# Kernel optimization log

Measured on AMD Instinct MI355X. Metric: run time of the kernel, lower is better.

The kernel has to match this reference:

```python
import jax, jax.numpy as jnp
import numpy as np

BS, SEQ, NV, DM, K = 128, 2048, 64, 512, 64
MAX_ITER, TOL = 10, 1e-4


def setup_inputs() -> dict:
    key = jax.random.key(0)
    k1, k2, k3, k4 = jax.random.split(key, 4)
    x = jax.random.normal(k1, (BS, SEQ, NV), jnp.float32)
    bound = 1.0 / np.sqrt(SEQ)
    W = jax.random.uniform(k2, (DM, SEQ), jnp.float32, -bound, bound)  # nn.Linear weight
    b = jax.random.uniform(k3, (DM,), jnp.float32, -bound, bound)
    centroids = jax.random.normal(k4, (K, DM), jnp.float32)  # kaiming-uniform-init param (random stand-in)
    return {"x": x, "W": W, "b": b, "centroids": centroids}


def _kmeans(x_emb, centroids):
    # x_emb: [N, DM]; fixed-length scan with a `done` flag emulating torch's tol break.
    N = x_emb.shape[0]
    x_sq = jnp.sum(x_emb * x_emb, axis=1, keepdims=True)  # [N,1]

    def body(state, _):
        cent, ids, done = state
        # squared euclidean distances (argmin-equivalent to cdist p=2)
        d2 = x_sq - 2.0 * (x_emb @ cent.T) + jnp.sum(cent * cent, axis=1)  # [N,K]
        new_ids = jnp.argmin(d2, axis=1)
        sums = jax.ops.segment_sum(x_emb, new_ids, num_segments=K)          # [K,DM]
        counts = jax.ops.segment_sum(jnp.ones((N,), x_emb.dtype), new_ids, num_segments=K)
        means = sums / jnp.maximum(counts, 1.0)[:, None]
        new_cent = jnp.where((counts > 0)[:, None], means, cent)  # empty cluster keeps old centroid
        shift = jnp.linalg.norm(new_cent - cent)
        cent_out = jnp.where(done, cent, new_cent)
        ids_out = jnp.where(done, ids, new_ids)
        done_out = done | (shift < TOL)
        return (cent_out, ids_out, done_out), None

    init = (centroids, jnp.zeros((N,), jnp.int32), jnp.array(False))
    (cent, ids, _), _ = jax.lax.scan(body, init, None, length=MAX_ITER)
    return ids, cent


def reference(x, W, b, centroids):
    # x: [bs, seq, n_vars] -> permute -> linear(seq->d_model) -> [bs*n_vars, d_model]
    xt = jnp.transpose(x, (0, 2, 1))                 # [bs, n_vars, seq]
    x_emb = (xt @ W.T + b).reshape(-1, DM)           # [bs*n_vars, d_model]
    ids, cent = _kmeans(x_emb, centroids)
    prob = jax.nn.one_hot(ids, K, dtype=jnp.float32).reshape(BS, NV, K)
    return prob, cent, x_emb
```

## Files before the change

kernel.cpp:

```cpp
#include <hip/hip_runtime.h>

#define SEQ 2048
#define NVAR 64
#define DMODEL 512
#define BSZ 128
#define KC 64
#define NPT (BSZ*NVAR)
#define MAXIT 10

typedef __bf16 bf16x8 __attribute__((ext_vector_type(8)));
typedef float f32x4 __attribute__((ext_vector_type(4)));

__device__ __forceinline__ void load_lds16(const void* g, void* l) {
  __builtin_amdgcn_global_load_lds((const __attribute__((address_space(1))) void*)g,
                                   (__attribute__((address_space(3))) void*)l, 16, 0, 0);
}

__device__ __forceinline__ unsigned short bf16_rn(float x) {
  unsigned int u = __float_as_uint(x);
  u += 0x7fffu + ((u >> 16) & 1u);
  return (unsigned short)(u >> 16);
}

__global__ __launch_bounds__(256) void prep_k(const float* __restrict__ x,
    unsigned short* __restrict__ Xh, unsigned short* __restrict__ Xl,
    const float* __restrict__ W, unsigned short* __restrict__ Wh,
    unsigned short* __restrict__ Wl) {
  __shared__ float tile[64 * 65];
  const int fid = blockIdx.x;
  const int t = threadIdx.x;

  if (fid < 1024) {
    int i = (fid * 256 + t) * 4;
    float4 v = *(const float4*)(W + i);
    ushort4 h, l;
    h.x = bf16_rn(v.x); l.x = bf16_rn(v.x - __uint_as_float((unsigned)h.x << 16));
    h.y = bf16_rn(v.y); l.y = bf16_rn(v.y - __uint_as_float((unsigned)h.y << 16));
    h.z = bf16_rn(v.z); l.z = bf16_rn(v.z - __uint_as_float((unsigned)h.z << 16));
    h.w = bf16_rn(v.w); l.w = bf16_rn(v.w - __uint_as_float((unsigned)h.w << 16));
    *(ushort4*)(Wh + i) = h;
    *(ushort4*)(Wl + i) = l;
  }

  const int k0 = (fid & 31) * 64;
  const int bs = fid >> 5;
  const float* xb = x + (size_t)bs * SEQ * NVAR + (size_t)k0 * NVAR;
  #pragma unroll
  for (int p = 0; p < 4; ++p) {
    int idx = t + 256 * p;
    int row = idx >> 4, c4 = (idx & 15) * 4;
    float4 v = *(const float4*)(xb + row * NVAR + c4);
    tile[row * 65 + c4 + 0] = v.x; tile[row * 65 + c4 + 1] = v.y;
    tile[row * 65 + c4 + 2] = v.z; tile[row * 65 + c4 + 3] = v.w;
  }
  __syncthreads();
  const int v = t >> 2;
  const int kc = (t & 3) * 16;
  unsigned short h[16], l[16];
  #pragma unroll
  for (int j = 0; j < 16; ++j) {
    float f = tile[(kc + j) * 65 + v];
    h[j] = bf16_rn(f);
    l[j] = bf16_rn(f - __uint_as_float((unsigned)h[j] << 16));
  }
  size_t off = (size_t)(bs * 64 + v) * SEQ + k0 + kc;
  *(uint4*)(Xh + off)     = *(uint4*)&h[0];
  *(uint4*)(Xh + off + 8) = *(uint4*)&h[8];
  *(uint4*)(Xl + off)     = *(uint4*)&l[0];
  *(uint4*)(Xl + off + 8) = *(uint4*)&l[8];
}

__global__ __launch_bounds__(256) void gemm_mfma(
    const unsigned short* __restrict__ Ah, const unsigned short* __restrict__ Al,
    const unsigned short* __restrict__ Bh, const unsigned short* __restrict__ Bl,
    const float* __restrict__ bias, float* __restrict__ emb) {
  __shared__ unsigned short sAh[32 * 64] __attribute__((aligned(16)));
  __shared__ unsigned short sAl[32 * 64] __attribute__((aligned(16)));
  __shared__ unsigned short sBh[256 * 64] __attribute__((aligned(16)));
  __shared__ unsigned short sBl[256 * 64] __attribute__((aligned(16)));
  const int t = threadIdx.x;
  const int w = t >> 6, lane = t & 63;
  const int m0 = blockIdx.x * 32;
  const int n0 = blockIdx.y * 256;
  const int wn = w * 64;
  const int lrow = lane >> 3, sl8 = lane & 7;
  const int csrc = sl8 ^ lrow;

  f32x4 acc[2][4];
  #pragma unroll
  for (int i = 0; i < 2; ++i)
    #pragma unroll
    for (int j = 0; j < 4; ++j) acc[i][j] = (f32x4){0.f, 0.f, 0.f, 0.f};

  for (int kt = 0; kt < SEQ; kt += 64) {
    __syncthreads();
    {
      const int r = w * 8 + lrow;
      const size_t ga = (size_t)(m0 + r) * SEQ + kt + csrc * 8;
      load_lds16(Ah + ga, &sAh[r * 64 + sl8 * 8]);
      load_lds16(Al + ga, &sAl[r * 64 + sl8 * 8]);
    }
    #pragma unroll
    for (int i = 0; i < 8; ++i) {
      const int r = w * 64 + i * 8 + lrow;
      const size_t gb = (size_t)(n0 + r) * SEQ + kt + csrc * 8;
      load_lds16(Bh + gb, &sBh[r * 64 + sl8 * 8]);
      load_lds16(Bl + gb, &sBl[r * 64 + sl8 * 8]);
    }
    __syncthreads();
    #pragma unroll
    for (int kk = 0; kk < 2; ++kk) {
      const int sl = ((kk * 4 + (lane >> 4)) ^ (lane & 7)) * 8;
      bf16x8 ah[2], al[2], bh[4], bl[4];
      #pragma unroll
      for (int mi = 0; mi < 2; ++mi) {
        int off = (mi * 16 + (lane & 15)) * 64 + sl;
        ah[mi] = *(const bf16x8*)&sAh[off];
        al[mi] = *(const bf16x8*)&sAl[off];
      }
      #pragma unroll
      for (int ni = 0; ni < 4; ++ni) {
        int off = (wn + ni * 16 + (lane & 15)) * 64 + sl;
        bh[ni] = *(const bf16x8*)&sBh[off];
        bl[ni] = *(const bf16x8*)&sBl[off];
      }
      #pragma unroll
      for (int mi = 0; mi < 2; ++mi)
        #pragma unroll
        for (int ni = 0; ni < 4; ++ni) {
          acc[mi][ni] = __builtin_amdgcn_mfma_f32_16x16x32_bf16(ah[mi], bh[ni], acc[mi][ni], 0, 0, 0);
          acc[mi][ni] = __builtin_amdgcn_mfma_f32_16x16x32_bf16(ah[mi], bl[ni], acc[mi][ni], 0, 0, 0);
          acc[mi][ni] = __builtin_amdgcn_mfma_f32_16x16x32_bf16(al[mi], bh[ni], acc[mi][ni], 0, 0, 0);
        }
    }
  }
  #pragma unroll
  for (int ni = 0; ni < 4; ++ni) {
    const int n = n0 + wn + ni * 16 + (lane & 15);
    const float bv = bias[n];
    #pragma unroll
    for (int mi = 0; mi < 2; ++mi) {
      const int m = m0 + mi * 16 + (lane >> 4) * 4;
      #pragma unroll
      for (int r = 0; r < 4; ++r)
        emb[(size_t)(m + r) * DMODEL + n] = acc[mi][ni][r] + bv;
    }
  }
}

__global__ __launch_bounds__(256) void gemm_emb(const float* __restrict__ x,
    const float* __restrict__ W, const float* __restrict__ bias,
    float* __restrict__ emb) {
  __shared__ float As[64][64];
  __shared__ float Ws[64][132];
  const int bs = blockIdx.y;
  const int n0 = blockIdx.x * 128;
  const int t = threadIdx.x;
  const int tx = t & 15, ty = t >> 4;
  float bv[8];
  #pragma unroll
  for (int j = 0; j < 8; ++j) bv[j] = bias[n0 + 8 * tx + j];
  float acc[4][8];
  #pragma unroll
  for (int i = 0; i < 4; ++i)
    #pragma unroll
    for (int j = 0; j < 8; ++j) acc[i][j] = 0.f;
  const float* xb = x + (size_t)bs * SEQ * NVAR;
  for (int k0 = 0; k0 < SEQ; k0 += 64) {
    __syncthreads();
    {
      const float4* src = (const float4*)(xb + (size_t)k0 * NVAR);
      float4* dst = (float4*)&As[0][0];
      #pragma unroll
      for (int r = 0; r < 4; ++r) dst[t + 256 * r] = src[t + 256 * r];
    }
    #pragma unroll
    for (int r = 0; r < 8; ++r) {
      int idx = t + 256 * r;
      int k4 = idx & 15, n = idx >> 4;
      float4 wv = *(const float4*)(W + (size_t)(n0 + n) * SEQ + k0 + 4 * k4);
      Ws[4 * k4 + 0][n] = wv.x; Ws[4 * k4 + 1][n] = wv.y;
      Ws[4 * k4 + 2][n] = wv.z; Ws[4 * k4 + 3][n] = wv.w;
    }
    __syncthreads();
    #pragma unroll 8
    for (int kk = 0; kk < 64; ++kk) {
      const float4 a  = *(const float4*)&As[kk][4 * ty];
      const float4 w0 = *(const float4*)&Ws[kk][8 * tx];
      const float4 w1 = *(const float4*)&Ws[kk][8 * tx + 4];
      const float av[4] = {a.x, a.y, a.z, a.w};
      const float wv[8] = {w0.x, w0.y, w0.z, w0.w, w1.x, w1.y, w1.z, w1.w};
      #pragma unroll
      for (int i = 0; i < 4; ++i)
        #pragma unroll
        for (int j = 0; j < 8; ++j)
          acc[i][j] = fmaf(av[i], wv[j], acc[i][j]);
    }
  }
  #pragma unroll
  for (int i = 0; i < 4; ++i) {
    int row = bs * NVAR + 4 * ty + i;
    float4 o0 = make_float4(acc[i][0] + bv[0], acc[i][1] + bv[1],
                            acc[i][2] + bv[2], acc[i][3] + bv[3]);
    float4 o1 = make_float4(acc[i][4] + bv[4], acc[i][5] + bv[5],
                            acc[i][6] + bv[6], acc[i][7] + bv[7]);
    *(float4*)(emb + (size_t)row * DMODEL + n0 + 8 * tx) = o0;
    *(float4*)(emb + (size_t)row * DMODEL + n0 + 8 * tx + 4) = o1;
  }
}

__global__ __launch_bounds__(256) void conv_et(const float* __restrict__ emb,
    unsigned short* __restrict__ Eh, unsigned short* __restrict__ El,
    unsigned short* __restrict__ Eth, unsigned short* __restrict__ Etl,
    const float* __restrict__ c0, float* __restrict__ cent,
    unsigned short* __restrict__ centh, unsigned short* __restrict__ centl,
    float* __restrict__ csq4, int* __restrict__ done,
    float* __restrict__ shift2, int* __restrict__ ticket) {
  __shared__ unsigned short Lh[64][72];
  __shared__ unsigned short Ll[64][72];
  __shared__ float red[256];
  const int d0 = blockIdx.x * 64;
  const int p0 = blockIdx.y * 64;
  const int t = threadIdx.x;
  #pragma unroll
  for (int q = 0; q < 2; ++q) {
    int idx = t + 256 * q;
    int r = idx >> 3, c = idx & 7;
    const float* src = emb + (size_t)(p0 + r) * DMODEL + d0 + c * 8;
    float4 v0 = *(const float4*)src;
    float4 v1 = *(const float4*)(src + 4);
    unsigned short h[8], l[8];
    const float vv[8] = {v0.x, v0.y, v0.z, v0.w, v1.x, v1.y, v1.z, v1.w};
    #pragma unroll
    for (int j = 0; j < 8; ++j) {
      h[j] = bf16_rn(vv[j]);
      l[j] = bf16_rn(vv[j] - __uint_as_float((unsigned)h[j] << 16));
    }
    size_t eo = (size_t)(p0 + r) * DMODEL + d0 + c * 8;
    *(uint4*)(Eh + eo) = *(uint4*)&h[0];
    *(uint4*)(El + eo) = *(uint4*)&l[0];
    *(uint4*)&Lh[r][c * 8] = *(uint4*)&h[0];
    *(uint4*)&Ll[r][c * 8] = *(uint4*)&l[0];
  }
  __syncthreads();
  #pragma unroll
  for (int q = 0; q < 2; ++q) {
    int idx = t + 256 * q;
    int dd = idx >> 3, pc = idx & 7;
    unsigned short h[8], l[8];
    #pragma unroll
    for (int j = 0; j < 8; ++j) {
      h[j] = Lh[pc * 8 + j][dd];
      l[j] = Ll[pc * 8 + j][dd];
    }
    size_t to = (size_t)(d0 + dd) * NPT + p0 + pc * 8;
    *(uint4*)(Eth + to) = *(uint4*)&h[0];
    *(uint4*)(Etl + to) = *(uint4*)&l[0];
  }

  const int fid = blockIdx.x + 8 * blockIdx.y;
  if (fid < KC) {
    const int k = fid;
    float v0, v1;
    {
      int d = t;
      v0 = c0[k * DMODEL + d];
      cent[k * DMODEL + d] = v0;
      unsigned short h = bf16_rn(v0);
      centh[k * DMODEL + d] = h;
      centl[k * DMODEL + d] = bf16_rn(v0 - __uint_as_float((unsigned)h << 16));
    }
    {
      int d = t + 256;
      v1 = c0[k * DMODEL + d];
      cent[k * DMODEL + d] = v1;
      unsigned short h = bf16_rn(v1);
      centh[k * DMODEL + d] = h;
      centl[k * DMODEL + d] = bf16_rn(v1 - __uint_as_float((unsigned)h << 16));
    }
    __syncthreads();
    red[t] = v0 * v0; __syncthreads();
    for (int s = 64; s > 0; s >>= 1) { if ((t & 127) < s) red[t] += red[t + s]; __syncthreads(); }
    if (t == 0)   csq4[0 * KC + k] = red[0];
    if (t == 128) csq4[1 * KC + k] = red[128];
    __syncthreads();
    red[t] = v1 * v1; __syncthreads();
    for (int s = 64; s > 0; s >>= 1) { if ((t & 127) < s) red[t] += red[t + s]; __syncthreads(); }
    if (t == 0)   csq4[2 * KC + k] = red[0];
    if (t == 128) csq4[3 * KC + k] = red[128];
    if (k == 0 && t < MAXIT) { shift2[t] = 0.f; ticket[t] = 0; }
    if (k == 0 && t == 31) *done = 0;
  }
}

__global__ __launch_bounds__(128) void k1_assign(
    const unsigned short* __restrict__ Eh, const unsigned short* __restrict__ El,
    const unsigned short* __restrict__ Ch, const unsigned short* __restrict__ Cl,
    const float* __restrict__ csq4, const int* __restrict__ done,
    int* __restrict__ ids, float* __restrict__ pcnt) {
  if (*done) return;
  __shared__ unsigned short sEh[32 * 64] __attribute__((aligned(16)));
  __shared__ unsigned short sEl[32 * 64] __attribute__((aligned(16)));
  __shared__ unsigned short sCh[64 * 64] __attribute__((aligned(16)));
  __shared__ unsigned short sCl[64 * 64] __attribute__((aligned(16)));
  __shared__ float Dmat[32][65];
  __shared__ float csq_l[64];
  __shared__ int cnt_l[64];
  const int t = threadIdx.x;
  const int w = t >> 6, lane = t & 63;
  const int p0 = blockIdx.x * 32;
  const int lrow = lane >> 3, sl8 = lane & 7;
  const int csrc = sl8 ^ lrow;
  if (t < 64) {
    csq_l[t] = csq4[t] + csq4[KC + t] + csq4[2 * KC + t] + csq4[3 * KC + t];
    cnt_l[t] = 0;
  }

  f32x4 acc[4];
  #pragma unroll
  for (int j = 0; j < 4; ++j) acc[j] = (f32x4){0.f, 0.f, 0.f, 0.f};

  for (int kt = 0; kt < DMODEL; kt += 64) {
    __syncthreads();
    #pragma unroll
    for (int i = 0; i < 2; ++i) {
      const int r = w * 16 + i * 8 + lrow;
      const size_t ga = (size_t)(p0 + r) * DMODEL + kt + csrc * 8;
      load_lds16(Eh + ga, &sEh[r * 64 + sl8 * 8]);
      load_lds16(El + ga, &sEl[r * 64 + sl8 * 8]);
    }
    #pragma unroll
    for (int i = 0; i < 4; ++i) {
      const int r = w * 32 + i * 8 + lrow;
      const size_t gc = (size_t)r * DMODEL + kt + csrc * 8;
      load_lds16(Ch + gc, &sCh[r * 64 + sl8 * 8]);
      load_lds16(Cl + gc, &sCl[r * 64 + sl8 * 8]);
    }
    __syncthreads();
    #pragma unroll
    for (int kk = 0; kk < 2; ++kk) {
      const int sl = ((kk * 4 + (lane >> 4)) ^ (lane & 7)) * 8;
      bf16x8 eh, el, ch[4], cl[4];
      {
        int off = (w * 16 + (lane & 15)) * 64 + sl;
        eh = *(const bf16x8*)&sEh[off];
        el = *(const bf16x8*)&sEl[off];
      }
      #pragma unroll
      for (int ni = 0; ni < 4; ++ni) {
        int off = (ni * 16 + (lane & 15)) * 64 + sl;
        ch[ni] = *(const bf16x8*)&sCh[off];
        cl[ni] = *(const bf16x8*)&sCl[off];
      }
      #pragma unroll
      for (int ni = 0; ni < 4; ++ni) {
        acc[ni] = __builtin_amdgcn_mfma_f32_16x16x32_bf16(eh, ch[ni], acc[ni], 0, 0, 0);
        acc[ni] = __builtin_amdgcn_mfma_f32_16x16x32_bf16(eh, cl[ni], acc[ni], 0, 0, 0);
        acc[ni] = __builtin_amdgcn_mfma_f32_16x16x32_bf16(el, ch[ni], acc[ni], 0, 0, 0);
      }
    }
  }
  #pragma unroll
  for (int ni = 0; ni < 4; ++ni) {
    const int p = w * 16 + (lane >> 4) * 4;
    const int k = ni * 16 + (lane & 15);
    const float csq = csq_l[k];
    #pragma unroll
    for (int r = 0; r < 4; ++r)
      Dmat[p + r][k] = csq - 2.f * acc[ni][r];
  }
  __syncthreads();
  if (t < 32) {
    float best = Dmat[t][0]; int bi = 0;
    #pragma unroll 8
    for (int k = 1; k < KC; ++k) {
      float v = Dmat[t][k];
      if (v < best) { best = v; bi = k; }
    }
    ids[p0 + t] = bi;
    atomicAdd(&cnt_l[bi], 1);
  }
  __syncthreads();
  if (t < 64) pcnt[blockIdx.x * KC + t] = (float)cnt_l[t];
}

__global__ __launch_bounds__(256) void k2_segsum(
    const unsigned short* __restrict__ Eth, const unsigned short* __restrict__ Etl,
    const int* __restrict__ ids, const int* __restrict__ done,
    float* __restrict__ psum) {
  if (*done) return;
  __shared__ unsigned short sOH[64 * 136] __attribute__((aligned(16)));
  __shared__ unsigned short sTh[128 * 64] __attribute__((aligned(16)));
  __shared__ unsigned short sTl[128 * 64] __attribute__((aligned(16)));
  __shared__ int ids_l[128];
  const int t = threadIdx.x;
  const int w = t >> 6, lane = t & 63;
  const int dq = blockIdx.x, g = blockIdx.y;
  const int lrow = lane >> 3, sl8 = lane & 7;
  const int csrc = sl8 ^ lrow;

  if (t < 128) ids_l[t] = ids[g * 128 + t];
  __syncthreads();
  #pragma unroll
  for (int q = 0; q < 4; ++q) {
    int c = t * 4 + q;
    int cl = c >> 4, pc = c & 15;
    unsigned short v[8];
    #pragma unroll
    for (int j = 0; j < 8; ++j)
      v[j] = (ids_l[pc * 8 + j] == cl) ? (unsigned short)0x3F80 : (unsigned short)0;
    *(uint4*)&sOH[cl * 136 + pc * 8] = *(uint4*)&v[0];
  }

  f32x4 acc[4][2];
  #pragma unroll
  for (int i = 0; i < 4; ++i)
    #pragma unroll
    for (int j = 0; j < 2; ++j) acc[i][j] = (f32x4){0.f, 0.f, 0.f, 0.f};

  for (int kt = 0; kt < 2; ++kt) {
    __syncthreads();
    #pragma unroll
    for (int i = 0; i < 4; ++i) {
      const int rr = w * 32 + i * 8 + lrow;
      const size_t gt = (size_t)(dq * 128 + rr) * NPT + g * 128 + kt * 64 + csrc * 8;
      load_lds16(Eth + gt, &sTh[rr * 64 + sl8 * 8]);
      load_lds16(Etl + gt, &sTl[rr * 64 + sl8 * 8]);
    }
    __syncthreads();
    #pragma unroll
    for (int kk = 0; kk < 2; ++kk) {
      const int quad = lane >> 4;
      const int poff = kt * 64 + kk * 32 + quad * 8;
      bf16x8 a[4], bh[2], bl[2];
      #pragma unroll
      for (int mi = 0; mi < 4; ++mi)
        a[mi] = *(const bf16x8*)&sOH[(mi * 16 + (lane & 15)) * 136 + poff];
      const int sl = ((kk * 4 + quad) ^ (lane & 7)) * 8;
      #pragma unroll
      for (int ni = 0; ni < 2; ++ni) {
        int off = (w * 32 + ni * 16 + (lane & 15)) * 64 + sl;
        bh[ni] = *(const bf16x8*)&sTh[off];
        bl[ni] = *(const bf16x8*)&sTl[off];
      }
      #pragma unroll
      for (int mi = 0; mi < 4; ++mi)
        #pragma unroll
        for (int ni = 0; ni < 2; ++ni) {
          acc[mi][ni] = __builtin_amdgcn_mfma_f32_16x16x32_bf16(a[mi], bh[ni], acc[mi][ni], 0, 0, 0);
          acc[mi][ni] = __builtin_amdgcn_mfma_f32_16x16x32_bf16(a[mi], bl[ni], acc[mi][ni], 0, 0, 0);
        }
    }
  }
  #pragma unroll
  for (int mi = 0; mi < 4; ++mi)
    #pragma unroll
    for (int ni = 0; ni < 2; ++ni) {
      const int cl = mi * 16 + (lane >> 4) * 4;
      const int d = dq * 128 + w * 32 + ni * 16 + (lane & 15);
      #pragma unroll
      for (int r = 0; r < 4; ++r)
        psum[((size_t)g * KC + cl + r) * DMODEL + d] = acc[mi][ni][r];
    }
}

__global__ __launch_bounds__(128) void k3_update(float* __restrict__ cent,
    unsigned short* __restrict__ centh, unsigned short* __restrict__ centl,
    const float* __restrict__ psum, const float* __restrict__ pcnt,
    int* __restrict__ done, float* __restrict__ csq4,
    float* __restrict__ shift2, int* __restrict__ ticket, int iter,
    const int* __restrict__ ids, float* __restrict__ out, int is_last) {
  const int dn = *done;
  const int bk = blockIdx.x & 63, dq = blockIdx.x >> 6;
  const int t = threadIdx.x;
  const int d = dq * 128 + t;
  __shared__ float red[128];
  __shared__ float cnt_s;
  float outv = 0.f;
  if (!dn) {
    red[t] = pcnt[(size_t)(2 * t) * KC + bk] + pcnt[(size_t)(2 * t + 1) * KC + bk];
    __syncthreads();
    for (int s = 64; s > 0; s >>= 1) { if (t < s) red[t] += red[t + s]; __syncthreads(); }
    if (t == 0) cnt_s = red[0];
    __syncthreads();
    const float count = cnt_s;
    float s = 0.f;
    #pragma unroll 16
    for (int g = 0; g < 64; ++g)
      s += psum[((size_t)g * KC + bk) * DMODEL + d];
    float oldv = cent[bk * DMODEL + d];
    float newv = (count > 0.f) ? (s / fmaxf(count, 1.f)) : oldv;
    cent[bk * DMODEL + d] = newv;
    unsigned short h = bf16_rn(newv);
    centh[bk * DMODEL + d] = h;
    centl[bk * DMODEL + d] = bf16_rn(newv - __uint_as_float((unsigned)h << 16));
    outv = newv;
    float df = newv - oldv;
    red[t] = df * df; __syncthreads();
    for (int s2 = 64; s2 > 0; s2 >>= 1) { if (t < s2) red[t] += red[t + s2]; __syncthreads(); }
    float tot_sh = red[0]; __syncthreads();
    red[t] = newv * newv; __syncthreads();
    for (int s2 = 64; s2 > 0; s2 >>= 1) { if (t < s2) red[t] += red[t + s2]; __syncthreads(); }
    if (t == 0) {
      csq4[dq * KC + bk] = red[0];
      atomicAdd(shift2 + iter, tot_sh);
      __threadfence();
      int tk = atomicAdd(ticket + iter, 1);
      if (tk == 255) {
        float tot = atomicAdd(shift2 + iter, 0.f);
        if (sqrtf(tot) < 1e-4f) *done = 1;
      }
    }
  } else {
    outv = cent[bk * DMODEL + d];
  }
  if (is_last) {
    out[(size_t)NPT * KC + bk * DMODEL + d] = outv;
    const int n = blockIdx.x * 32 + (t >> 2);
    const int k0 = (t & 3) * 16;
    const int idn = ids[n];
    #pragma unroll
    for (int j = 0; j < 4; ++j) {
      float4 v;
      v.x = (idn == k0 + j * 4 + 0) ? 1.f : 0.f;
      v.y = (idn == k0 + j * 4 + 1) ? 1.f : 0.f;
      v.z = (idn == k0 + j * 4 + 2) ? 1.f : 0.f;
      v.w = (idn == k0 + j * 4 + 3) ? 1.f : 0.f;
      *(float4*)(out + (size_t)n * KC + k0 + j * 4) = v;
    }
  }
}

extern "C" void kernel_launch(void* const* d_in, const int* in_sizes, int n_in,
                              void* d_out, int out_size, void* d_ws, size_t ws_size,
                              hipStream_t stream) {
  const float* x    = (const float*)d_in[0];
  const float* W    = (const float*)d_in[1];
  const float* bias = (const float*)d_in[2];
  const float* c0   = (const float*)d_in[3];
  float* out = (float*)d_out;
  float* emb_out = out + NPT * KC + KC * DMODEL;

  char* ws = (char*)d_ws;
  unsigned short* Ehi  = (unsigned short*)(ws + 0);
  unsigned short* Elo  = (unsigned short*)(ws + 8388608);
  unsigned short* Eth  = (unsigned short*)(ws + 16777216);
  unsigned short* Etl  = (unsigned short*)(ws + 25165824);
  float* psum    = (float*)(ws + 33554432);
  float* cent    = (float*)(ws + 41943040);
  unsigned short* centh = (unsigned short*)(ws + 42074112);
  unsigned short* centl = (unsigned short*)(ws + 42139648);
  float* csq4    = (float*)(ws + 42205184);
  float* shift2  = (float*)(ws + 42206208);
  int*   ticket  = (int*)(ws + 42206272);
  int*   done_f  = (int*)(ws + 42206336);
  float* pcnt    = (float*)(ws + 42206400);
  int*   ids     = (int*)(ws + 42271936);
  unsigned short* Xh = (unsigned short*)(ws + 0);
  unsigned short* Xl = (unsigned short*)(ws + 33554432);
  unsigned short* Wh = (unsigned short*)(ws + 67108864);
  unsigned short* Wl = (unsigned short*)(ws + 69206016);
  const size_t need_fast = 71303168;
  (void)n_in; (void)in_sizes; (void)out_size;

  if (ws_size >= need_fast) {
    prep_k<<<4096, 256, 0, stream>>>(x, Xh, Xl, W, Wh, Wl);
    gemm_mfma<<<dim3(256, 2), 256, 0, stream>>>(Xh, Xl, Wh, Wl, bias, emb_out);
  } else {
    gemm_emb<<<dim3(4, BSZ), 256, 0, stream>>>(x, W, bias, emb_out);
  }
  conv_et<<<dim3(8, 128), 256, 0, stream>>>(emb_out, Ehi, Elo, Eth, Etl,
                                            c0, cent, centh, centl, csq4,
                                            done_f, shift2, ticket);
  for (int it = 0; it < MAXIT; ++it) {
    k1_assign<<<256, 128, 0, stream>>>(Ehi, Elo, centh, centl, csq4, done_f, ids, pcnt);
    k2_segsum<<<dim3(4, 64), 256, 0, stream>>>(Eth, Etl, ids, done_f, psum);
    k3_update<<<256, 128, 0, stream>>>(cent, centh, centl, psum, pcnt, done_f,
                                       csq4, shift2, ticket, it,
                                       ids, out, it == MAXIT - 1);
  }
}
```

Before: 482.8 us.

## Retile embedding GEMM to 64x128 and widen K-steps in k-means kernels

The embedding GEMM block tile changes from 32x256 to 64x128 with a 2x2 wave grid. This balances A and B reuse and cuts LDS and global traffic per MFMA, and the grid is adjusted to match. The assign kernel now loads two 64-wide K slices per barrier pair, halving the number of sync rounds. The segment-sum kernel issues all transposed-embedding tile loads up front, overlapping them with one-hot construction and removing a barrier loop. LDS footprint grows in both k-means kernels, which may lower occupancy.

Result: faster. 451.6 us (-6.5%).

```diff
diff --git a/kernel.cpp b/kernel.cpp
--- a/kernel.cpp
+++ b/kernel.cpp
@@ -74,15 +74,15 @@
     const unsigned short* __restrict__ Ah, const unsigned short* __restrict__ Al,
     const unsigned short* __restrict__ Bh, const unsigned short* __restrict__ Bl,
     const float* __restrict__ bias, float* __restrict__ emb) {
-  __shared__ unsigned short sAh[32 * 64] __attribute__((aligned(16)));
-  __shared__ unsigned short sAl[32 * 64] __attribute__((aligned(16)));
-  __shared__ unsigned short sBh[256 * 64] __attribute__((aligned(16)));
-  __shared__ unsigned short sBl[256 * 64] __attribute__((aligned(16)));
+  __shared__ unsigned short sAh[64 * 64] __attribute__((aligned(16)));
+  __shared__ unsigned short sAl[64 * 64] __attribute__((aligned(16)));
+  __shared__ unsigned short sBh[128 * 64] __attribute__((aligned(16)));
+  __shared__ unsigned short sBl[128 * 64] __attribute__((aligned(16)));
   const int t = threadIdx.x;
   const int w = t >> 6, lane = t & 63;
-  const int m0 = blockIdx.x * 32;
-  const int n0 = blockIdx.y * 256;
-  const int wn = w * 64;
+  const int m0 = blockIdx.x * 64;
+  const int n0 = blockIdx.y * 128;
+  const int wr = w >> 1, wc = w & 1;
   const int lrow = lane >> 3, sl8 = lane & 7;
   const int csrc = sl8 ^ lrow;
 
@@ -94,15 +94,16 @@
 
   for (int kt = 0; kt < SEQ; kt += 64) {
     __syncthreads();
-    {
-      const int r = w * 8 + lrow;
+    #pragma unroll
+    for (int i = 0; i < 2; ++i) {
+      const int r = w * 16 + i * 8 + lrow;
       const size_t ga = (size_t)(m0 + r) * SEQ + kt + csrc * 8;
       load_lds16(Ah + ga, &sAh[r * 64 + sl8 * 8]);
       load_lds16(Al + ga, &sAl[r * 64 + sl8 * 8]);
     }
     #pragma unroll
-    for (int i = 0; i < 8; ++i) {
-      const int r = w * 64 + i * 8 + lrow;
+    for (int i = 0; i < 4; ++i) {
+      const int r = w * 32 + i * 8 + lrow;
       const size_t gb = (size_t)(n0 + r) * SEQ + kt + csrc * 8;
       load_lds16(Bh + gb, &sBh[r * 64 + sl8 * 8]);
       load_lds16(Bl + gb, &sBl[r * 64 + sl8 * 8]);
@@ -114,13 +115,13 @@
       bf16x8 ah[2], al[2], bh[4], bl[4];
       #pragma unroll
       for (int mi = 0; mi < 2; ++mi) {
-        int off = (mi * 16 + (lane & 15)) * 64 + sl;
+        int off = (wr * 32 + mi * 16 + (lane & 15)) * 64 + sl;
         ah[mi] = *(const bf16x8*)&sAh[off];
         al[mi] = *(const bf16x8*)&sAl[off];
       }
       #pragma unroll
       for (int ni = 0; ni < 4; ++ni) {
-        int off = (wn + ni * 16 + (lane & 15)) * 64 + sl;
+        int off = (wc * 64 + ni * 16 + (lane & 15)) * 64 + sl;
         bh[ni] = *(const bf16x8*)&sBh[off];
         bl[ni] = *(const bf16x8*)&sBl[off];
       }
@@ -136,11 +137,11 @@
   }
   #pragma unroll
   for (int ni = 0; ni < 4; ++ni) {
-    const int n = n0 + wn + ni * 16 + (lane & 15);
+    const int n = n0 + wc * 64 + ni * 16 + (lane & 15);
     const float bv = bias[n];
     #pragma unroll
     for (int mi = 0; mi < 2; ++mi) {
-      const int m = m0 + mi * 16 + (lane >> 4) * 4;
+      const int m = m0 + wr * 32 + mi * 16 + (lane >> 4) * 4;
       #pragma unroll
       for (int r = 0; r < 4; ++r)
         emb[(size_t)(m + r) * DMODEL + n] = acc[mi][ni][r] + bv;
@@ -299,10 +300,10 @@
     const float* __restrict__ csq4, const int* __restrict__ done,
     int* __restrict__ ids, float* __restrict__ pcnt) {
   if (*done) return;
-  __shared__ unsigned short sEh[32 * 64] __attribute__((aligned(16)));
-  __shared__ unsigned short sEl[32 * 64] __attribute__((aligned(16)));
-  __shared__ unsigned short sCh[64 * 64] __attribute__((aligned(16)));
-  __shared__ unsigned short sCl[64 * 64] __attribute__((aligned(16)));
+  __shared__ unsigned short sEh[2][32 * 64] __attribute__((aligned(16)));
+  __shared__ unsigned short sEl[2][32 * 64] __attribute__((aligned(16)));
+  __shared__ unsigned short sCh[2][64 * 64] __attribute__((aligned(16)));
+  __shared__ unsigned short sCl[2][64 * 64] __attribute__((aligned(16)));
   __shared__ float Dmat[32][65];
   __shared__ float csq_l[64];
   __shared__ int cnt_l[64];
@@ -320,37 +321,41 @@
   #pragma unroll
   for (int j = 0; j < 4; ++j) acc[j] = (f32x4){0.f, 0.f, 0.f, 0.f};
 
-  for (int kt = 0; kt < DMODEL; kt += 64) {
-    __syncthreads();
-    #pragma unroll
-    for (int i = 0; i < 2; ++i) {
-      const int r = w * 16 + i * 8 + lrow;
-      const size_t ga = (size_t)(p0 + r) * DMODEL + kt + csrc * 8;
-      load_lds16(Eh + ga, &sEh[r * 64 + sl8 * 8]);
-      load_lds16(El + ga, &sEl[r * 64 + sl8 * 8]);
-    }
-    #pragma unroll
-    for (int i = 0; i < 4; ++i) {
-      const int r = w * 32 + i * 8 + lrow;
-      const size_t gc = (size_t)r * DMODEL + kt + csrc * 8;
-      load_lds16(Ch + gc, &sCh[r * 64 + sl8 * 8]);
-      load_lds16(Cl + gc, &sCl[r * 64 + sl8 * 8]);
-    }
-    __syncthreads();
-    #pragma unroll
-    for (int kk = 0; kk < 2; ++kk) {
-      const int sl = ((kk * 4 + (lane >> 4)) ^ (lane & 7)) * 8;
+  for (int kt = 0; kt < DMODEL; kt += 128) {
+    __syncthreads();
+    #pragma unroll
+    for (int h = 0; h < 2; ++h) {
+      #pragma unroll
+      for (int i = 0; i < 2; ++i) {
+        const int r = w * 16 + i * 8 + lrow;
+        const size_t ga = (size_t)(p0 + r) * DMODEL + kt + h * 64 + csrc * 8;
+        load_lds16(Eh + ga, &sEh[h][r * 64 + sl8 * 8]);
+        load_lds16(El + ga, &sEl[h][r * 64 + sl8 * 8]);
+      }
+      #pragma unroll
+      for (int i = 0; i < 4; ++i) {
+        const int r = w * 32 + i * 8 + lrow;
+        const size_t gc = (size_t)r * DMODEL + kt + h * 64 + csrc * 8;
+        load_lds16(Ch + gc, &sCh[h][r * 64 + sl8 * 8]);
+        load_lds16(Cl + gc, &sCl[h][r * 64 + sl8 * 8]);
+      }
+    }
+    __syncthreads();
+    #pragma unroll
+    for (int kk4 = 0; kk4 < 4; ++kk4) {
+      const int h = kk4 >> 1, kk2 = kk4 & 1;
+      const int sl = ((kk2 * 4 + (lane >> 4)) ^ (lane & 7)) * 8;
       bf16x8 eh, el, ch[4], cl[4];
       {
         int off = (w * 16 + (lane & 15)) * 64 + sl;
-        eh = *(const bf16x8*)&sEh[off];
-        el = *(const bf16x8*)&sEl[off];
+        eh = *(const bf16x8*)&sEh[h][off];
+        el = *(const bf16x8*)&sEl[h][off];
       }
       #pragma unroll
       for (int ni = 0; ni < 4; ++ni) {
         int off = (ni * 16 + (lane & 15)) * 64 + sl;
-        ch[ni] = *(const bf16x8*)&sCh[off];
-        cl[ni] = *(const bf16x8*)&sCl[off];
+        ch[ni] = *(const bf16x8*)&sCh[h][off];
+        cl[ni] = *(const bf16x8*)&sCl[h][off];
       }
       #pragma unroll
       for (int ni = 0; ni < 4; ++ni) {
@@ -390,8 +395,8 @@
     float* __restrict__ psum) {
   if (*done) return;
   __shared__ unsigned short sOH[64 * 136] __attribute__((aligned(16)));
-  __shared__ unsigned short sTh[128 * 64] __attribute__((aligned(16)));
-  __shared__ unsigned short sTl[128 * 64] __attribute__((aligned(16)));
+  __shared__ unsigned short sTh[2][128 * 64] __attribute__((aligned(16)));
+  __shared__ unsigned short sTl[2][128 * 64] __attribute__((aligned(16)));
   __shared__ int ids_l[128];
   const int t = threadIdx.x;
   const int w = t >> 6, lane = t & 63;
@@ -402,6 +407,16 @@
   if (t < 128) ids_l[t] = ids[g * 128 + t];
   __syncthreads();
   #pragma unroll
+  for (int h = 0; h < 2; ++h) {
+    #pragma unroll
+    for (int i = 0; i < 4; ++i) {
+      const int rr = w * 32 + i * 8 + lrow;
+      const size_t gt = (size_t)(dq * 128 + rr) * NPT + g * 128 + h * 64 + csrc * 8;
+      load_lds16(Eth + gt, &sTh[h][rr * 64 + sl8 * 8]);
+      load_lds16(Etl + gt, &sTl[h][rr * 64 + sl8 * 8]);
+    }
+  }
+  #pragma unroll
   for (int q = 0; q < 4; ++q) {
     int c = t * 4 + q;
     int cl = c >> 4, pc = c & 15;
@@ -418,39 +433,30 @@
     #pragma unroll
     for (int j = 0; j < 2; ++j) acc[i][j] = (f32x4){0.f, 0.f, 0.f, 0.f};
 
-  for (int kt = 0; kt < 2; ++kt) {
-    __syncthreads();
-    #pragma unroll
-    for (int i = 0; i < 4; ++i) {
-      const int rr = w * 32 + i * 8 + lrow;
-      const size_t gt = (size_t)(dq * 128 + rr) * NPT + g * 128 + kt * 64 + csrc * 8;
-      load_lds16(Eth + gt, &sTh[rr * 64 + sl8 * 8]);
-      load_lds16(Etl + gt, &sTl[rr * 64 + sl8 * 8]);
-    }
-    __syncthreads();
-    #pragma unroll
-    for (int kk = 0; kk < 2; ++kk) {
-      const int quad = lane >> 4;
-      const int poff = kt * 64 + kk * 32 + quad * 8;
-      bf16x8 a[4], bh[2], bl[2];
-      #pragma unroll
-      for (int mi = 0; mi < 4; ++mi)
-        a[mi] = *(const bf16x8*)&sOH[(mi * 16 + (lane & 15)) * 136 + poff];
-      const int sl = ((kk * 4 + quad) ^ (lane & 7)) * 8;
+  __syncthreads();
+  #pragma unroll
+  for (int kk4 = 0; kk4 < 4; ++kk4) {
+    const int h = kk4 >> 1, kk2 = kk4 & 1;
+    const int quad = lane >> 4;
+    const int poff = kk4 * 32 + quad * 8;
+    bf16x8 a[4], bh[2], bl[2];
+    #pragma unroll
+    for (int mi = 0; mi < 4; ++mi)
+      a[mi] = *(const bf16x8*)&sOH[(mi * 16 + (lane & 15)) * 136 + poff];
+    const int sl = ((kk2 * 4 + quad) ^ (lane & 7)) * 8;
+    #pragma unroll
+    for (int ni = 0; ni < 2; ++ni) {
+      int off = (w * 32 + ni * 16 + (lane & 15)) * 64 + sl;
+      bh[ni] = *(const bf16x8*)&sTh[h][off];
+      bl[ni] = *(const bf16x8*)&sTl[h][off];
+    }
+    #pragma unroll
+    for (int mi = 0; mi < 4; ++mi)
       #pragma unroll
       for (int ni = 0; ni < 2; ++ni) {
-        int off = (w * 32 + ni * 16 + (lane & 15)) * 64 + sl;
-        bh[ni] = *(const bf16x8*)&sTh[off];
-        bl[ni] = *(const bf16x8*)&sTl[off];
-      }
-      #pragma unroll
-      for (int mi = 0; mi < 4; ++mi)
-        #pragma unroll
-        for (int ni = 0; ni < 2; ++ni) {
-          acc[mi][ni] = __builtin_amdgcn_mfma_f32_16x16x32_bf16(a[mi], bh[ni], acc[mi][ni], 0, 0, 0);
-          acc[mi][ni] = __builtin_amdgcn_mfma_f32_16x16x32_bf16(a[mi], bl[ni], acc[mi][ni], 0, 0, 0);
-        }
-    }
+        acc[mi][ni] = __builtin_amdgcn_mfma_f32_16x16x32_bf16(a[mi], bh[ni], acc[mi][ni], 0, 0, 0);
+        acc[mi][ni] = __builtin_amdgcn_mfma_f32_16x16x32_bf16(a[mi], bl[ni], acc[mi][ni], 0, 0, 0);
+      }
   }
   #pragma unroll
   for (int mi = 0; mi < 4; ++mi)
@@ -565,7 +571,7 @@
 
   if (ws_size >= need_fast) {
     prep_k<<<4096, 256, 0, stream>>>(x, Xh, Xl, W, Wh, Wl);
-    gemm_mfma<<<dim3(256, 2), 256, 0, stream>>>(Xh, Xl, Wh, Wl, bias, emb_out);
+    gemm_mfma<<<dim3(128, 4), 256, 0, stream>>>(Xh, Xl, Wh, Wl, bias, emb_out);
   } else {
     gemm_emb<<<dim3(4, BSZ), 256, 0, stream>>>(x, W, bias, emb_out);
   }
```
